# Optimization experiments

Hardware: AMD Instinct MI355X
Metric: run time of the kernel (lower is better)

The kernel has to match this reference:

```python
import jax, jax.numpy as jnp
import numpy as np

EPS = 1e-8

def _gn1(x, w, b):
    # GroupNorm(num_groups=1): normalize each sample over (C, T), per-channel affine.
    mean = jnp.mean(x, axis=(1, 2), keepdims=True)
    var = jnp.mean((x - mean) ** 2, axis=(1, 2), keepdims=True)
    xn = (x - mean) * jax.lax.rsqrt(var + EPS)
    return xn * w[None, :, None] + b[None, :, None]

def _film(h, e, gw, gb, bw, bb):
    # gamma/beta: Linear -> ReLU (dropout is identity in eval), broadcast over time.
    gamma = jax.nn.relu(e @ gw.T + gb)  # [B, C]
    beta = jax.nn.relu(e @ bw.T + bb)   # [B, C]
    return gamma[:, :, None] * h + beta[:, :, None]

def setup_inputs() -> dict:
    key = jax.random.key(0)
    ks = jax.random.split(key, 16)
    B, C, T = 16, 256, 16000
    s = lambda k, shape, scale: jax.random.normal(k, shape, dtype=jnp.float32) * scale
    return {
        "x": s(ks[0], (B, C, T), 1.0),
        "cue": s(ks[1], (B, 512), 1.0),
        "gn_a_w": jnp.ones((C,), jnp.float32), "gn_a_b": jnp.zeros((C,), jnp.float32),
        "gn_n_w": jnp.ones((C,), jnp.float32), "gn_n_b": jnp.zeros((C,), jnp.float32),
        "f1g_w": s(ks[2], (C, 512), 0.04), "f1g_b": jnp.zeros((C,), jnp.float32),
        "f1b_w": s(ks[3], (C, 512), 0.04), "f1b_b": jnp.zeros((C,), jnp.float32),
        "ln1_w": jnp.ones((C,), jnp.float32), "ln1_b": jnp.zeros((C,), jnp.float32),
        "conv1_w": s(ks[4], (128, C), 0.06),
        "cds_w": s(ks[5], (256, 512), 0.04),
        "f2g_w": s(ks[6], (128, 256), 0.06), "f2g_b": jnp.zeros((128,), jnp.float32),
        "f2b_w": s(ks[7], (128, 256), 0.06), "f2b_b": jnp.zeros((128,), jnp.float32),
        "ln2_w": jnp.ones((128,), jnp.float32), "ln2_b": jnp.zeros((128,), jnp.float32),
        "conv2_w": s(ks[8], (256, 128), 0.08),
    }

def reference(x, cue, gn_a_w, gn_a_b, gn_n_w, gn_n_b, f1g_w, f1g_b, f1b_w, f1b_b,
              ln1_w, ln1_b, conv1_w, cds_w, f2g_w, f2g_b, f2b_w, f2b_b,
              ln2_w, ln2_b, conv2_w):
    x = _gn1(x, gn_a_w, gn_a_b)                 # norm_audio (GroupNorm(1, C))
    x = _gn1(x, gn_n_w, gn_n_b)                 # norm (GroupNorm(1, C))
    x = _film(x, cue, f1g_w, f1g_b, f1b_w, f1b_b) + x  # film1 + residual
    x = _gn1(x, ln1_w, ln1_b)                   # layer_norm1
    x = jnp.einsum('bct,oc->bot', x, conv1_w)   # 1x1 Conv1d, no bias -> [B,128,T]
    cue2 = jax.nn.relu(cue @ cds_w.T)           # cue_down_sample2 -> [B,256]
    x = _film(x, cue2, f2g_w, f2g_b, f2b_w, f2b_b) + x  # film2 + residual
    x = _gn1(x, ln2_w, ln2_b)                   # layer_norm2
    x = jnp.einsum('bct,oc->bot', x, conv2_w)   # 1x1 Conv1d -> [B,256,T]
    return x
```

## Files before the change

### kernel.cpp

```cpp
#include <hip/hip_runtime.h>
#include <hip/hip_bf16.h>
#include <hip/hip_fp16.h>

#define T_LEN   16000
#define NB      16
#define NTT     250
#define NTB     125
#define EPSV    1e-8f

typedef _Float16 f16x8 __attribute__((ext_vector_type(8)));
typedef float    f32x4 __attribute__((ext_vector_type(4)));

__device__ __forceinline__ ushort f2h(float f) {
    _Float16 h = (_Float16)f;
    return *(ushort*)&h;
}
__device__ __forceinline__ float f4c(const float4& v, int i) {
    return i == 0 ? v.x : i == 1 ? v.y : i == 2 ? v.z : v.w;
}
__device__ __forceinline__ void gld16(const ushort* g, ushort* l) {
    __builtin_amdgcn_global_load_lds(
        (const __attribute__((address_space(1))) uint*)g,
        (__attribute__((address_space(3))) uint*)l, 16, 0, 0);
}
__device__ __forceinline__ float waveRed64(float v) {
    #pragma unroll
    for (int m = 1; m <= 32; m <<= 1) v += __shfl_xor(v, m, 64);
    return v;
}
__device__ __forceinline__ float4 ntload4(const float* p) {
    f32x4 v = __builtin_nontemporal_load((const f32x4*)p);
    return make_float4(v[0], v[1], v[2], v[3]);
}

__global__ __launch_bounds__(256) void kP1F(
    const float* __restrict__ x, ushort* __restrict__ Xp,
    float* __restrict__ sp, float* __restrict__ qp,
    const float* __restrict__ cue,
    const float* __restrict__ f1g_w, const float* __restrict__ f1g_b,
    const float* __restrict__ f1b_w, const float* __restrict__ f1b_b,
    const float* __restrict__ cds_w,
    float* __restrict__ G1, float* __restrict__ B1, float* __restrict__ CUE2)
{
    const int bid = blockIdx.x;
    if (bid < 256) {
        const int c = bid;
        const int lane = threadIdx.x & 63, w = threadIdx.x >> 6;
        const float4 wg0 = *(const float4*)(f1g_w + c*512 + lane*8);
        const float4 wg1 = *(const float4*)(f1g_w + c*512 + lane*8 + 4);
        const float4 wb0 = *(const float4*)(f1b_w + c*512 + lane*8);
        const float4 wb1 = *(const float4*)(f1b_w + c*512 + lane*8 + 4);
        const float4 wc0 = *(const float4*)(cds_w + c*512 + lane*8);
        const float4 wc1 = *(const float4*)(cds_w + c*512 + lane*8 + 4);
        #pragma unroll
        for (int bb = 0; bb < 4; ++bb) {
            const int b = w*4 + bb;
            const float4 u0 = *(const float4*)(cue + b*512 + lane*8);
            const float4 u1 = *(const float4*)(cue + b*512 + lane*8 + 4);
            float g = 0.f, bt = 0.f, cv = 0.f;
            #pragma unroll
            for (int i = 0; i < 4; ++i) {
                g  = fmaf(f4c(u0,i), f4c(wg0,i), g);  g  = fmaf(f4c(u1,i), f4c(wg1,i), g);
                bt = fmaf(f4c(u0,i), f4c(wb0,i), bt); bt = fmaf(f4c(u1,i), f4c(wb1,i), bt);
                cv = fmaf(f4c(u0,i), f4c(wc0,i), cv); cv = fmaf(f4c(u1,i), f4c(wc1,i), cv);
            }
            g = waveRed64(g); bt = waveRed64(bt); cv = waveRed64(cv);
            if (lane == 0) {
                G1[b*256 + c]   = fmaxf(g + f1g_b[c], 0.f) + 1.f;
                B1[b*256 + c]   = fmaxf(bt + f1b_b[c], 0.f);
                CUE2[b*256 + c] = fmaxf(cv, 0.f);
            }
        }
        return;
    }

    const int pb = bid - 256;
    const int b = pb / NTT, tt = pb % NTT;
    const int t0 = tt * 64;
    const int tid = threadIdx.x;
    const int cq = tid >> 2, jq = tid & 3;
    __shared__ __align__(16) ushort Hs[256][68];

    #pragma unroll
    for (int cc = 0; cc < 4; ++cc) {
        const int c = cc*64 + cq;
        float s4 = 0.f, q4 = 0.f;
        #pragma unroll
        for (int i = 0; i < 4; ++i) {
            const int ts = (jq + i*4)*4;
            const float4 v = ntload4(x + ((size_t)(b*256 + c))*T_LEN + t0 + ts);
            s4 += v.x + v.y + v.z + v.w;
            q4 += v.x*v.x + v.y*v.y + v.z*v.z + v.w*v.w;
            const ushort h0 = f2h(v.x), h1 = f2h(v.y), h2 = f2h(v.z), h3 = f2h(v.w);
            uint2 pk;
            pk.x = (uint)h0 | ((uint)h1 << 16);
            pk.y = (uint)h2 | ((uint)h3 << 16);
            *(uint2*)&Hs[c][ts] = pk;
        }
        s4 += __shfl_xor(s4, 1, 4); s4 += __shfl_xor(s4, 2, 4);
        q4 += __shfl_xor(q4, 1, 4); q4 += __shfl_xor(q4, 2, 4);
        if (jq == 0) {
            sp[((size_t)b*NTT + tt)*256 + c] = s4;
            qp[((size_t)b*NTT + tt)*256 + c] = q4;
        }
    }
    __syncthreads();
    ushort* dst = Xp + ((size_t)(b*NTT + tt)*4)*4096;
    #pragma unroll
    for (int k = 0; k < 8; ++k) {
        const int d  = tid + k*256;
        const int kc = d >> 9, r = d & 511;
        const int t  = r >> 3, us = r & 7;
        const int u  = us ^ (t & 7);
        const int c0 = kc*64 + u*8;
        uint4 val;
        val.x = (uint)Hs[c0+0][t] | ((uint)Hs[c0+1][t] << 16);
        val.y = (uint)Hs[c0+2][t] | ((uint)Hs[c0+3][t] << 16);
        val.z = (uint)Hs[c0+4][t] | ((uint)Hs[c0+5][t] << 16);
        val.w = (uint)Hs[c0+6][t] | ((uint)Hs[c0+7][t] << 16);
        *(uint4*)(dst + (size_t)d*8) = val;
    }
}

__global__ __launch_bounds__(256) void kR_reduce(
    const float* __restrict__ sp, const float* __restrict__ qp,
    float* __restrict__ s1, float* __restrict__ q1)
{
    const int cg = blockIdx.x, b = blockIdx.y;
    const int ci = threadIdx.x & 31, ig = threadIdx.x >> 5;
    const int c = cg*32 + ci;
    float s = 0.f, q = 0.f;
    for (int i = ig; i < NTT; i += 8) {
        s += sp[((size_t)b*NTT + i)*256 + c];
        q += qp[((size_t)b*NTT + i)*256 + c];
    }
    __shared__ float rs[8][32], rq[8][32];
    rs[ig][ci] = s; rq[ig][ci] = q;
    __syncthreads();
    if (threadIdx.x < 32) {
        float ss = 0.f, qq = 0.f;
        #pragma unroll
        for (int g = 0; g < 8; ++g) { ss += rs[g][threadIdx.x]; qq += rq[g][threadIdx.x]; }
        s1[b*256 + cg*32 + threadIdx.x] = ss;
        q1[b*256 + cg*32 + threadIdx.x] = qq;
    }
}

__device__ __forceinline__ float blockSum256(float v, float* red)
{
    #pragma unroll
    for (int off = 32; off; off >>= 1) v += __shfl_down(v, off, 64);
    __syncthreads();
    if ((threadIdx.x & 63) == 0) red[threadIdx.x >> 6] = v;
    __syncthreads();
    return red[0] + red[1] + red[2] + red[3];
}

__global__ __launch_bounds__(256) void kBM(
    const float* __restrict__ s1, const float* __restrict__ q1,
    const float* __restrict__ gn_a_w, const float* __restrict__ gn_a_b,
    const float* __restrict__ gn_n_w, const float* __restrict__ gn_n_b,
    const float* __restrict__ G1, const float* __restrict__ B1,
    const float* __restrict__ ln1_w, const float* __restrict__ ln1_b,
    const float* __restrict__ CUE2,
    const float* __restrict__ f2g_w, const float* __restrict__ f2g_b,
    const float* __restrict__ f2b_w, const float* __restrict__ f2b_b,
    const float* __restrict__ conv1_w,
    float* __restrict__ a4o, float* __restrict__ G2,
    float* __restrict__ E, ushort* __restrict__ Msf)
{
    const int b = blockIdx.x;
    const int c = threadIdx.x;
    __shared__ float red[4];
    __shared__ float sa4[256], sd4[256], sc2[256], sg2[16];

    const float sc = s1[b*256 + c];
    const float qc = q1[b*256 + c];

    const float Ninv = 1.f / (256.f * 16000.f);
    const float Tf = 16000.f;

    float S  = blockSum256(sc, red);
    float Q  = blockSum256(qc, red);
    float mu1 = S * Ninv;
    float var1 = Q * Ninv - mu1 * mu1;
    float r1 = rsqrtf(var1 + EPSV);
    float a1 = gn_a_w[c] * r1;
    float d1 = gn_a_b[c] - mu1 * r1 * gn_a_w[c];

    float S2 = blockSum256(a1*sc + Tf*d1, red);
    float Q2 = blockSum256(a1*a1*qc + 2.f*a1*d1*sc + Tf*d1*d1, red);
    float mu2 = S2 * Ninv;
    float var2 = Q2 * Ninv - mu2 * mu2;
    float r2 = rsqrtf(var2 + EPSV);
    float wn = gn_n_w[c];
    float a2 = wn * r2 * a1;
    float d2 = wn * r2 * (d1 - mu2) + gn_n_b[c];

    const float g1 = G1[b*256 + c];
    const float b1 = B1[b*256 + c];
    float a3 = g1 * a2;
    float d3 = g1 * d2 + b1;

    float S3 = blockSum256(a3*sc + Tf*d3, red);
    float Q3 = blockSum256(a3*a3*qc + 2.f*a3*d3*sc + Tf*d3*d3, red);
    float mu3 = S3 * Ninv;
    float var3 = Q3 * Ninv - mu3 * mu3;
    float r3 = rsqrtf(var3 + EPSV);
    float w1 = ln1_w[c];
    const float a4v = w1 * r3 * a3;
    const float d4v = w1 * r3 * (d3 - mu3) + ln1_b[c];
    sa4[c] = a4v;
    sd4[c] = d4v;
    a4o[b*256 + c] = a4v;
    sc2[c] = CUE2[b*256 + c];
    __syncthreads();

    const int oi = c >> 4, l16 = c & 15;
    for (int og = 0; og < 8; ++og) {
        const int o = og*16 + oi;
        float g = 0.f, bt = 0.f, ed = 0.f;
        #pragma unroll
        for (int q = 0; q < 4; ++q) {
            const int k0 = l16*16 + q*4;
            const float4 a  = *(const float4*)(f2g_w  + o*256 + k0);
            const float4 bb = *(const float4*)(f2b_w  + o*256 + k0);
            const float4 cc = *(const float4*)(conv1_w + o*256 + k0);
            const float4 u  = *(const float4*)(&sc2[k0]);
            const float4 dd = *(const float4*)(&sd4[k0]);
            #pragma unroll
            for (int i = 0; i < 4; ++i) {
                g  = fmaf(f4c(u,i),  f4c(a,i),  g);
                bt = fmaf(f4c(u,i),  f4c(bb,i), bt);
                ed = fmaf(f4c(dd,i), f4c(cc,i), ed);
            }
        }
        #pragma unroll
        for (int m = 1; m <= 8; m <<= 1) {
            g  += __shfl_xor(g, m, 16);
            bt += __shfl_xor(bt, m, 16);
            ed += __shfl_xor(ed, m, 16);
        }
        if (l16 == 0) {
            const float G2v = fmaxf(g + f2g_b[o], 0.f) + 1.f;
            const float B2v = fmaxf(bt + f2b_b[o], 0.f);
            G2[b*128 + o] = G2v;
            E[b*128 + o]  = G2v * ed + B2v;
            sg2[oi] = G2v;
        }
        __syncthreads();
        const float av = sa4[c];
        #pragma unroll
        for (int i = 0; i < 16; ++i) {
            const int oo = og*16 + i;
            Msf[((size_t)b*128 + oo)*256 + c] = f2h(sg2[i] * conv1_w[oo*256 + c] * av);
        }
        __syncthreads();
    }
}

__global__ __launch_bounds__(256) void kC_gemm(
    const ushort* __restrict__ Xp, const ushort* __restrict__ Msf,
    const float* __restrict__ E,
    float* __restrict__ s2p, float* __restrict__ q2p)
{
    const int tb = blockIdx.x, b = blockIdx.y;
    const int tid = threadIdx.x, lane = tid & 63, w = tid >> 6;
    const int wo = w >> 1, wt = w & 1;
    const int sub = lane >> 4, li = lane & 15;
    const int o0 = wo * 64;
    __shared__ __align__(16) ushort Bs[32768];
    __shared__ float sSp[2][128], sQp[2][128];

    const ushort* src = Xp + ((size_t)(b*NTT + 2*tb)*4)*4096;
    const ushort* mp  = Msf + (size_t)b*128*256;

    f32x4 acc[4][4];
    #pragma unroll
    for (int i = 0; i < 4; ++i)
        #pragma unroll
        for (int jx = 0; jx < 4; ++jx) acc[i][jx] = (f32x4){0.f,0.f,0.f,0.f};

    #pragma unroll
    for (int m = 0; m < 16; ++m) {
        const int off = m*2048 + w*512;
        gld16(src + off + lane*8, &Bs[off]);
    }
    __syncthreads();

    #pragma unroll
    for (int ks = 0; ks < 8; ++ks) {
        const int kc = ks >> 1;
        const int uo = (ks & 1)*4 + sub;
        f16x8 xf[4];
        #pragma unroll
        for (int ft = 0; ft < 4; ++ft) {
            const int tl = ft*16 + li;
            xf[ft] = *(const f16x8*)&Bs[(wt*4 + kc)*4096 + tl*64 + (uo ^ (tl & 7))*8];
        }
        const int k8 = kc*64 + (ks & 1)*32 + 8*sub;
        #pragma unroll
        for (int fo = 0; fo < 4; ++fo) {
            const f16x8 mf = *(const f16x8*)(mp + (size_t)(o0 + fo*16 + li)*256 + k8);
            #pragma unroll
            for (int ft = 0; ft < 4; ++ft)
                acc[ft][fo] = __builtin_amdgcn_mfma_f32_16x16x32_f16(xf[ft], mf, acc[ft][fo], 0, 0, 0);
        }
    }

    #pragma unroll
    for (int fo = 0; fo < 4; ++fo) {
        const int o = o0 + fo*16 + li;
        const float ev = E[b*128 + o];
        float sv = 0.f, qv = 0.f;
        #pragma unroll
        for (int ft = 0; ft < 4; ++ft)
            #pragma unroll
            for (int r = 0; r < 4; ++r) {
                const float z = acc[ft][fo][r] + ev;
                sv += z; qv += z*z;
            }
        sv += __shfl_xor(sv, 16, 64); sv += __shfl_xor(sv, 32, 64);
        qv += __shfl_xor(qv, 16, 64); qv += __shfl_xor(qv, 32, 64);
        if (sub == 0) { sSp[wt][o] = sv; sQp[wt][o] = qv; }
    }
    __syncthreads();
    if (tid < 128) {
        s2p[((size_t)b*NTB + tb)*128 + tid] = sSp[0][tid] + sSp[1][tid];
        q2p[((size_t)b*NTB + tb)*128 + tid] = sQp[0][tid] + sQp[1][tid];
    }
}

__global__ __launch_bounds__(256) void kD2_buildF(
    const float* __restrict__ s2p, const float* __restrict__ q2p,
    const float* __restrict__ ln2_w, const float* __restrict__ ln2_b,
    const float* __restrict__ Ev,
    const float* __restrict__ a4, const float* __restrict__ G2,
    const float* __restrict__ conv1_w, const float* __restrict__ conv2_w,
    ushort* __restrict__ Fsf, float* __restrict__ h)
{
    const int b = blockIdx.y, pg = blockIdx.x;
    const int tid = threadIdx.x;
    __shared__ float Qs[32][128];
    __shared__ float sA2[128], sAE[128];
    __shared__ float rS[2], rQ[2];

    float s = 0.f, qq = 0.f;
    if (tid < 128) {
        for (int tb = 0; tb < NTB; ++tb) {
            s  += s2p[((size_t)b*NTB + tb)*128 + tid];
            qq += q2p[((size_t)b*NTB + tb)*128 + tid];
        }
        float S = s, Q = qq;
        #pragma unroll
        for (int off = 32; off; off >>= 1) {
            S += __shfl_down(S, off, 64);
            Q += __shfl_down(Q, off, 64);
        }
        if ((tid & 63) == 0) { rS[tid >> 6] = S; rQ[tid >> 6] = Q; }
    }
    __syncthreads();
    const float N2inv = 1.f / (128.f * 16000.f);
    const float mu  = (rS[0] + rS[1]) * N2inv;
    const float var = (rQ[0] + rQ[1]) * N2inv - mu * mu;
    const float r = rsqrtf(var + EPSV);
    if (tid < 128) {
        const float a2v = ln2_w[tid] * r;
        const float d2v = ln2_b[tid] - mu * ln2_w[tid] * r;
        sA2[tid] = a2v;
        sAE[tid] = a2v * Ev[b*128 + tid] + d2v;
    }
    __syncthreads();

    #pragma unroll
    for (int k = 0; k < 16; ++k) {
        const int idx = tid + k*256;
        const int p = idx >> 7, o = idx & 127;
        Qs[p][o] = conv2_w[(pg*32 + p)*128 + o] * sA2[o] * G2[b*128 + o];
    }
    __syncthreads();
    float acc[32];
    #pragma unroll
    for (int p = 0; p < 32; ++p) acc[p] = 0.f;
    for (int o = 0; o < 128; ++o) {
        const float mv = conv1_w[o*256 + tid];
        #pragma unroll
        for (int p = 0; p < 32; ++p) acc[p] = fmaf(Qs[p][o], mv, acc[p]);
    }
    const float a = a4[b*256 + tid];
    #pragma unroll
    for (int p = 0; p < 32; ++p) {
        const size_t idx = ((size_t)b*256 + pg*32 + p)*256 + tid;
        Fsf[idx] = f2h(acc[p] * a);
    }
    if (tid < 32) {
        const int p = pg*32 + tid;
        float hv = 0.f;
        for (int o = 0; o < 128; ++o)
            hv += conv2_w[p*128 + o] * sAE[o];
        h[b*256 + p] = hv;
    }
}

__global__ __launch_bounds__(256) void kE_gemm(
    const ushort* __restrict__ Xp, const ushort* __restrict__ Fsf,
    const float* __restrict__ h, float* __restrict__ out)
{
    const int tt = blockIdx.x, b = blockIdx.y;
    const int tid = threadIdx.x, lane = tid & 63, w = tid >> 6;
    const int sub = lane >> 4, li = lane & 15;
    const int o0 = w * 64, t0 = tt * 64;
    __shared__ __align__(16) ushort Bs[16384];

    const ushort* src = Xp + ((size_t)(b*NTT + tt)*4)*4096;
    const ushort* fp  = Fsf + (size_t)b*65536;

    f32x4 acc[4][4];
    #pragma unroll
    for (int i = 0; i < 4; ++i)
        #pragma unroll
        for (int jx = 0; jx < 4; ++jx) acc[i][jx] = (f32x4){0.f,0.f,0.f,0.f};

    #pragma unroll
    for (int m = 0; m < 8; ++m) {
        const int off = m*2048 + w*512;
        gld16(src + off + lane*8, &Bs[off]);
    }
    __syncthreads();

    #pragma unroll
    for (int ks = 0; ks < 8; ++ks) {
        const int kc = ks >> 1;
        const int uo = (ks & 1)*4 + sub;
        f16x8 xf[4];
        #pragma unroll
        for (int ft = 0; ft < 4; ++ft) {
            const int tl = ft*16 + li;
            xf[ft] = *(const f16x8*)&Bs[kc*4096 + tl*64 + (uo ^ (tl & 7))*8];
        }
        const int k8 = kc*64 + (ks & 1)*32 + 8*sub;
        #pragma unroll
        for (int fo = 0; fo < 4; ++fo) {
            const f16x8 ff = *(const f16x8*)(fp + (size_t)(o0 + fo*16 + li)*256 + k8);
            #pragma unroll
            for (int ft = 0; ft < 4; ++ft)
                acc[ft][fo] = __builtin_amdgcn_mfma_f32_16x16x32_f16(xf[ft], ff, acc[ft][fo], 0, 0, 0);
        }
    }

    #pragma unroll
    for (int fo = 0; fo < 4; ++fo) {
        const int o = o0 + fo*16 + li;
        const float hv = h[b*256 + o];
        float* obase = out + ((size_t)(b*256 + o))*T_LEN + t0;
        #pragma unroll
        for (int ft = 0; ft < 4; ++ft) {
            f32x4 v;
            v[0] = acc[ft][fo][0] + hv;
            v[1] = acc[ft][fo][1] + hv;
            v[2] = acc[ft][fo][2] + hv;
            v[3] = acc[ft][fo][3] + hv;
            __builtin_nontemporal_store(v, (f32x4*)(obase + ft*16 + sub*4));
        }
    }
}

extern "C" void kernel_launch(void* const* d_in, const int* in_sizes, int n_in,
                              void* d_out, int out_size, void* d_ws, size_t ws_size,
                              hipStream_t stream)
{
    const float* x       = (const float*)d_in[0];
    const float* cue     = (const float*)d_in[1];
    const float* gn_a_w  = (const float*)d_in[2];
    const float* gn_a_b  = (const float*)d_in[3];
    const float* gn_n_w  = (const float*)d_in[4];
    const float* gn_n_b  = (const float*)d_in[5];
    const float* f1g_w   = (const float*)d_in[6];
    const float* f1g_b   = (const float*)d_in[7];
    const float* f1b_w   = (const float*)d_in[8];
    const float* f1b_b   = (const float*)d_in[9];
    const float* ln1_w   = (const float*)d_in[10];
    const float* ln1_b   = (const float*)d_in[11];
    const float* conv1_w = (const float*)d_in[12];
    const float* cds_w   = (const float*)d_in[13];
    const float* f2g_w   = (const float*)d_in[14];
    const float* f2g_b   = (const float*)d_in[15];
    const float* f2b_w   = (const float*)d_in[16];
    const float* f2b_b   = (const float*)d_in[17];
    const float* ln2_w   = (const float*)d_in[18];
    const float* ln2_b   = (const float*)d_in[19];
    const float* conv2_w = (const float*)d_in[20];
    float* out = (float*)d_out;

    float* ws = (float*)d_ws;
    float*  sp   = ws;
    float*  qp   = ws + 1024000;
    float*  G1   = ws + 2048000;
    float*  B1   = ws + 2052096;
    float*  CUE2 = ws + 2056192;
    float*  G2   = ws + 2060288;
    float*  a4   = ws + 2062336;
    float*  E    = ws + 2066432;
    float*  h    = ws + 2068480;
    float*  s1   = ws + 2072576;
    float*  q1   = ws + 2076672;
    float*  s2p  = ws + 2080768;
    float*  q2p  = ws + 2336768;
    ushort* Msf  = (ushort*)(ws + 2592768);
    ushort* Fsf  = (ushort*)(ws + 2854912);
    ushort* Xp   = (ushort*)(ws + 3379200);

    kP1F<<<256 + NTT*NB, 256, 0, stream>>>(x, Xp, sp, qp,
        cue, f1g_w, f1g_b, f1b_w, f1b_b, cds_w, G1, B1, CUE2);

    kR_reduce<<<dim3(8, NB), 256, 0, stream>>>(sp, qp, s1, q1);

    kBM<<<NB, 256, 0, stream>>>(s1, q1, gn_a_w, gn_a_b, gn_n_w, gn_n_b,
                                G1, B1, ln1_w, ln1_b, CUE2,
                                f2g_w, f2g_b, f2b_w, f2b_b, conv1_w,
                                a4, G2, E, Msf);

    kC_gemm<<<dim3(NTB, NB), 256, 0, stream>>>(Xp, Msf, E, s2p, q2p);

    kD2_buildF<<<dim3(8, NB), 256, 0, stream>>>(s2p, q2p, ln2_w, ln2_b, E,
                                                a4, G2, conv1_w, conv2_w,
                                                Fsf, h);

    kE_gemm<<<dim3(NTT, NB), 256, 0, stream>>>(Xp, Fsf, h, out);
}
```

Baseline: 317.2 us.

## Split kBM into stats and parallel M-build, compute sum analytically, split kE_gemm outputs

The serial 16-block kBM kernel is split into a stats kernel and a kM2 kernel that spreads the per-output-group work over 8x16 blocks. The per-channel sum for layer_norm2 is now computed analytically from conv1_w, a4 and s1 instead of being accumulated in the GEMM epilogue, which removes the s2p writes and their reduction. kE_gemm is split across twice as many blocks, each covering 128 output channels, to raise occupancy. The costs are one extra launch and the X tiles being loaded twice in kE.

```diff
diff --git a/kernel.cpp b/kernel.cpp
--- a/kernel.cpp
+++ b/kernel.cpp
@@ -156,23 +156,17 @@
     return red[0] + red[1] + red[2] + red[3];
 }
 
-__global__ __launch_bounds__(256) void kBM(
+__global__ __launch_bounds__(256) void kBM_stats(
     const float* __restrict__ s1, const float* __restrict__ q1,
     const float* __restrict__ gn_a_w, const float* __restrict__ gn_a_b,
     const float* __restrict__ gn_n_w, const float* __restrict__ gn_n_b,
     const float* __restrict__ G1, const float* __restrict__ B1,
     const float* __restrict__ ln1_w, const float* __restrict__ ln1_b,
-    const float* __restrict__ CUE2,
-    const float* __restrict__ f2g_w, const float* __restrict__ f2g_b,
-    const float* __restrict__ f2b_w, const float* __restrict__ f2b_b,
-    const float* __restrict__ conv1_w,
-    float* __restrict__ a4o, float* __restrict__ G2,
-    float* __restrict__ E, ushort* __restrict__ Msf)
+    float* __restrict__ a4o, float* __restrict__ d4o)
 {
     const int b = blockIdx.x;
     const int c = threadIdx.x;
     __shared__ float red[4];
-    __shared__ float sa4[256], sd4[256], sc2[256], sg2[16];
 
     const float sc = s1[b*256 + c];
     const float qc = q1[b*256 + c];
@@ -208,61 +202,70 @@
     float var3 = Q3 * Ninv - mu3 * mu3;
     float r3 = rsqrtf(var3 + EPSV);
     float w1 = ln1_w[c];
-    const float a4v = w1 * r3 * a3;
-    const float d4v = w1 * r3 * (d3 - mu3) + ln1_b[c];
-    sa4[c] = a4v;
-    sd4[c] = d4v;
-    a4o[b*256 + c] = a4v;
-    sc2[c] = CUE2[b*256 + c];
-    __syncthreads();
-
-    const int oi = c >> 4, l16 = c & 15;
-    for (int og = 0; og < 8; ++og) {
-        const int o = og*16 + oi;
-        float g = 0.f, bt = 0.f, ed = 0.f;
-        #pragma unroll
-        for (int q = 0; q < 4; ++q) {
-            const int k0 = l16*16 + q*4;
-            const float4 a  = *(const float4*)(f2g_w  + o*256 + k0);
-            const float4 bb = *(const float4*)(f2b_w  + o*256 + k0);
-            const float4 cc = *(const float4*)(conv1_w + o*256 + k0);
-            const float4 u  = *(const float4*)(&sc2[k0]);
-            const float4 dd = *(const float4*)(&sd4[k0]);
-            #pragma unroll
-            for (int i = 0; i < 4; ++i) {
-                g  = fmaf(f4c(u,i),  f4c(a,i),  g);
-                bt = fmaf(f4c(u,i),  f4c(bb,i), bt);
-                ed = fmaf(f4c(dd,i), f4c(cc,i), ed);
-            }
-        }
-        #pragma unroll
-        for (int m = 1; m <= 8; m <<= 1) {
-            g  += __shfl_xor(g, m, 16);
-            bt += __shfl_xor(bt, m, 16);
-            ed += __shfl_xor(ed, m, 16);
-        }
-        if (l16 == 0) {
-            const float G2v = fmaxf(g + f2g_b[o], 0.f) + 1.f;
-            const float B2v = fmaxf(bt + f2b_b[o], 0.f);
-            G2[b*128 + o] = G2v;
-            E[b*128 + o]  = G2v * ed + B2v;
-            sg2[oi] = G2v;
-        }
-        __syncthreads();
-        const float av = sa4[c];
-        #pragma unroll
-        for (int i = 0; i < 16; ++i) {
-            const int oo = og*16 + i;
-            Msf[((size_t)b*128 + oo)*256 + c] = f2h(sg2[i] * conv1_w[oo*256 + c] * av);
-        }
-        __syncthreads();
+    a4o[b*256 + c] = w1 * r3 * a3;
+    d4o[b*256 + c] = w1 * r3 * (d3 - mu3) + ln1_b[c];
+}
+
+__global__ __launch_bounds__(256) void kM2(
+    const float* __restrict__ CUE2,
+    const float* __restrict__ f2g_w, const float* __restrict__ f2g_b,
+    const float* __restrict__ f2b_w, const float* __restrict__ f2b_b,
+    const float* __restrict__ conv1_w,
+    const float* __restrict__ a4, const float* __restrict__ d4,
+    float* __restrict__ G2, float* __restrict__ E, ushort* __restrict__ Msf)
+{
+    const int og = blockIdx.x, b = blockIdx.y;
+    const int tid = threadIdx.x;
+    __shared__ float sc2[256], sa4[256], sd4[256], sg2[16];
+    sc2[tid] = CUE2[b*256 + tid];
+    sa4[tid] = a4[b*256 + tid];
+    sd4[tid] = d4[b*256 + tid];
+    __syncthreads();
+
+    const int oi = tid >> 4, l16 = tid & 15;
+    const int o = og*16 + oi;
+    float g = 0.f, bt = 0.f, ed = 0.f;
+    #pragma unroll
+    for (int q = 0; q < 4; ++q) {
+        const int k0 = l16*16 + q*4;
+        const float4 a  = *(const float4*)(f2g_w  + o*256 + k0);
+        const float4 bb = *(const float4*)(f2b_w  + o*256 + k0);
+        const float4 c  = *(const float4*)(conv1_w + o*256 + k0);
+        const float4 u  = *(const float4*)(&sc2[k0]);
+        const float4 dd = *(const float4*)(&sd4[k0]);
+        #pragma unroll
+        for (int i = 0; i < 4; ++i) {
+            g  = fmaf(f4c(u,i),  f4c(a,i),  g);
+            bt = fmaf(f4c(u,i),  f4c(bb,i), bt);
+            ed = fmaf(f4c(dd,i), f4c(c,i),  ed);
+        }
+    }
+    #pragma unroll
+    for (int m = 1; m <= 8; m <<= 1) {
+        g  += __shfl_xor(g, m, 16);
+        bt += __shfl_xor(bt, m, 16);
+        ed += __shfl_xor(ed, m, 16);
+    }
+    if (l16 == 0) {
+        const float G2v = fmaxf(g + f2g_b[o], 0.f) + 1.f;
+        const float B2v = fmaxf(bt + f2b_b[o], 0.f);
+        G2[b*128 + o] = G2v;
+        E[b*128 + o]  = G2v * ed + B2v;
+        sg2[oi] = G2v;
+    }
+    __syncthreads();
+    const float av = sa4[tid];
+    #pragma unroll
+    for (int i = 0; i < 16; ++i) {
+        const int oo = og*16 + i;
+        Msf[((size_t)b*128 + oo)*256 + tid] = f2h(sg2[i] * conv1_w[oo*256 + tid] * av);
     }
 }
 
 __global__ __launch_bounds__(256) void kC_gemm(
     const ushort* __restrict__ Xp, const ushort* __restrict__ Msf,
     const float* __restrict__ E,
-    float* __restrict__ s2p, float* __restrict__ q2p)
+    float* __restrict__ q2p)
 {
     const int tb = blockIdx.x, b = blockIdx.y;
     const int tid = threadIdx.x, lane = tid & 63, w = tid >> 6;
@@ -270,7 +273,7 @@
     const int sub = lane >> 4, li = lane & 15;
     const int o0 = wo * 64;
     __shared__ __align__(16) ushort Bs[32768];
-    __shared__ float sSp[2][128], sQp[2][128];
+    __shared__ float sQp[2][128];
 
     const ushort* src = Xp + ((size_t)(b*NTT + 2*tb)*4)*4096;
     const ushort* mp  = Msf + (size_t)b*128*256;
@@ -312,46 +315,54 @@
     for (int fo = 0; fo < 4; ++fo) {
         const int o = o0 + fo*16 + li;
         const float ev = E[b*128 + o];
-        float sv = 0.f, qv = 0.f;
+        float qv = 0.f;
         #pragma unroll
         for (int ft = 0; ft < 4; ++ft)
             #pragma unroll
             for (int r = 0; r < 4; ++r) {
                 const float z = acc[ft][fo][r] + ev;
-                sv += z; qv += z*z;
+                qv += z*z;
             }
-        sv += __shfl_xor(sv, 16, 64); sv += __shfl_xor(sv, 32, 64);
         qv += __shfl_xor(qv, 16, 64); qv += __shfl_xor(qv, 32, 64);
-        if (sub == 0) { sSp[wt][o] = sv; sQp[wt][o] = qv; }
-    }
-    __syncthreads();
-    if (tid < 128) {
-        s2p[((size_t)b*NTB + tb)*128 + tid] = sSp[0][tid] + sSp[1][tid];
+        if (sub == 0) sQp[wt][o] = qv;
+    }
+    __syncthreads();
+    if (tid < 128)
         q2p[((size_t)b*NTB + tb)*128 + tid] = sQp[0][tid] + sQp[1][tid];
-    }
 }
 
 __global__ __launch_bounds__(256) void kD2_buildF(
-    const float* __restrict__ s2p, const float* __restrict__ q2p,
+    const float* __restrict__ q2p,
     const float* __restrict__ ln2_w, const float* __restrict__ ln2_b,
     const float* __restrict__ Ev,
     const float* __restrict__ a4, const float* __restrict__ G2,
+    const float* __restrict__ s1,
     const float* __restrict__ conv1_w, const float* __restrict__ conv2_w,
     ushort* __restrict__ Fsf, float* __restrict__ h)
 {
     const int b = blockIdx.y, pg = blockIdx.x;
     const int tid = threadIdx.x;
     __shared__ float Qs[32][128];
-    __shared__ float sA2[128], sAE[128];
+    __shared__ float sA2[128], sAE[128], sAS[256];
     __shared__ float rS[2], rQ[2];
 
-    float s = 0.f, qq = 0.f;
+    sAS[tid] = a4[b*256 + tid] * s1[b*256 + tid];
+    __syncthreads();
+
+    float s2v = 0.f, qq = 0.f;
     if (tid < 128) {
-        for (int tb = 0; tb < NTB; ++tb) {
-            s  += s2p[((size_t)b*NTB + tb)*128 + tid];
+        float dot = 0.f;
+        #pragma unroll 4
+        for (int c4 = 0; c4 < 64; ++c4) {
+            const float4 cw = *(const float4*)(conv1_w + tid*256 + c4*4);
+            const float4 as = *(const float4*)(&sAS[c4*4]);
+            dot = fmaf(cw.x, as.x, dot); dot = fmaf(cw.y, as.y, dot);
+            dot = fmaf(cw.z, as.z, dot); dot = fmaf(cw.w, as.w, dot);
+        }
+        s2v = G2[b*128 + tid] * dot + 16000.f * Ev[b*128 + tid];
+        for (int tb = 0; tb < NTB; ++tb)
             qq += q2p[((size_t)b*NTB + tb)*128 + tid];
-        }
-        float S = s, Q = qq;
+        float S = s2v, Q = qq;
         #pragma unroll
         for (int off = 32; off; off >>= 1) {
             S += __shfl_down(S, off, 64);
@@ -406,20 +417,22 @@
     const ushort* __restrict__ Xp, const ushort* __restrict__ Fsf,
     const float* __restrict__ h, float* __restrict__ out)
 {
-    const int tt = blockIdx.x, b = blockIdx.y;
+    const int tt = blockIdx.x;
+    const int b = blockIdx.y >> 1;
+    const int o_base = (blockIdx.y & 1) * 128;
     const int tid = threadIdx.x, lane = tid & 63, w = tid >> 6;
     const int sub = lane >> 4, li = lane & 15;
-    const int o0 = w * 64, t0 = tt * 64;
+    const int o0 = o_base + w * 32, t0 = tt * 64;
     __shared__ __align__(16) ushort Bs[16384];
 
     const ushort* src = Xp + ((size_t)(b*NTT + tt)*4)*4096;
     const ushort* fp  = Fsf + (size_t)b*65536;
 
-    f32x4 acc[4][4];
+    f32x4 acc[4][2];
     #pragma unroll
     for (int i = 0; i < 4; ++i)
         #pragma unroll
-        for (int jx = 0; jx < 4; ++jx) acc[i][jx] = (f32x4){0.f,0.f,0.f,0.f};
+        for (int jx = 0; jx < 2; ++jx) acc[i][jx] = (f32x4){0.f,0.f,0.f,0.f};
 
     #pragma unroll
     for (int m = 0; m < 8; ++m) {
@@ -440,7 +453,7 @@
         }
         const int k8 = kc*64 + (ks & 1)*32 + 8*sub;
         #pragma unroll
-        for (int fo = 0; fo < 4; ++fo) {
+        for (int fo = 0; fo < 2; ++fo) {
             const f16x8 ff = *(const f16x8*)(fp + (size_t)(o0 + fo*16 + li)*256 + k8);
             #pragma unroll
             for (int ft = 0; ft < 4; ++ft)
@@ -449,7 +462,7 @@
     }
 
     #pragma unroll
-    for (int fo = 0; fo < 4; ++fo) {
+    for (int fo = 0; fo < 2; ++fo) {
         const int o = o0 + fo*16 + li;
         const float hv = h[b*256 + o];
         float* obase = out + ((size_t)(b*256 + o))*T_LEN + t0;
@@ -500,31 +513,32 @@
     float*  CUE2 = ws + 2056192;
     float*  G2   = ws + 2060288;
     float*  a4   = ws + 2062336;
-    float*  E    = ws + 2066432;
-    float*  h    = ws + 2068480;
-    float*  s1   = ws + 2072576;
-    float*  q1   = ws + 2076672;
-    float*  s2p  = ws + 2080768;
-    float*  q2p  = ws + 2336768;
-    ushort* Msf  = (ushort*)(ws + 2592768);
-    ushort* Fsf  = (ushort*)(ws + 2854912);
-    ushort* Xp   = (ushort*)(ws + 3379200);
+    float*  d4   = ws + 2066432;
+    float*  E    = ws + 2070528;
+    float*  h    = ws + 2072576;
+    float*  s1   = ws + 2076672;
+    float*  q1   = ws + 2080768;
+    float*  q2p  = ws + 2084864;
+    ushort* Msf  = (ushort*)(ws + 2340864);
+    ushort* Fsf  = (ushort*)(ws + 2603008);
+    ushort* Xp   = (ushort*)(ws + 3127296);
 
     kP1F<<<256 + NTT*NB, 256, 0, stream>>>(x, Xp, sp, qp,
         cue, f1g_w, f1g_b, f1b_w, f1b_b, cds_w, G1, B1, CUE2);
 
     kR_reduce<<<dim3(8, NB), 256, 0, stream>>>(sp, qp, s1, q1);
 
-    kBM<<<NB, 256, 0, stream>>>(s1, q1, gn_a_w, gn_a_b, gn_n_w, gn_n_b,
-                                G1, B1, ln1_w, ln1_b, CUE2,
-                                f2g_w, f2g_b, f2b_w, f2b_b, conv1_w,
-                                a4, G2, E, Msf);
-
-    kC_gemm<<<dim3(NTB, NB), 256, 0, stream>>>(Xp, Msf, E, s2p, q2p);
-
-    kD2_buildF<<<dim3(8, NB), 256, 0, stream>>>(s2p, q2p, ln2_w, ln2_b, E,
-                                                a4, G2, conv1_w, conv2_w,
+    kBM_stats<<<NB, 256, 0, stream>>>(s1, q1, gn_a_w, gn_a_b, gn_n_w, gn_n_b,
+                                      G1, B1, ln1_w, ln1_b, a4, d4);
+
+    kM2<<<dim3(8, NB), 256, 0, stream>>>(CUE2, f2g_w, f2g_b, f2b_w, f2b_b,
+                                         conv1_w, a4, d4, G2, E, Msf);
+
+    kC_gemm<<<dim3(NTB, NB), 256, 0, stream>>>(Xp, Msf, E, q2p);
+
+    kD2_buildF<<<dim3(8, NB), 256, 0, stream>>>(q2p, ln2_w, ln2_b, E,
+                                                a4, G2, s1, conv1_w, conv2_w,
                                                 Fsf, h);
 
-    kE_gemm<<<dim3(NTT, NB), 256, 0, stream>>>(Xp, Fsf, h, out);
-}
+    kE_gemm<<<dim3(NTT, NB*2), 256, 0, stream>>>(Xp, Fsf, h, out);
+}
```

Measured after the change: 306.5 us (median of 2 runs). 1.03x faster.
